# Kernel optimization log

Measured on AMD Instinct MI355X. Metric: run time of the kernel, lower is better.

The kernel has to match this reference:

```python
import jax, jax.numpy as jnp
import numpy as np

N, F, DEG, C = 20000, 64, 16, 16   # nodes, features, in-degree incl. self loop, classes
E = N * (DEG - 1)                   # regular (non-self-loop) edges


def setup_inputs() -> dict:
    key = jax.random.key(0)
    ks = jax.random.split(key, 12)
    x = jax.random.normal(ks[0], (N, F), dtype=jnp.float32)
    src = jax.random.randint(ks[1], (E,), 0, N, dtype=jnp.int32)
    dst = jnp.repeat(jnp.arange(N, dtype=jnp.int32), DEG - 1)  # exactly DEG-1 in-edges/node
    edge_index = jnp.stack([src, dst])
    s = 1.0 / np.sqrt(F)
    params = {}
    for i, kw, kb in ((1, ks[2], ks[3]), (2, ks[4], ks[5]), (3, ks[6], ks[7])):
        params[f"W{i}"] = jax.random.normal(kw, (F, F), dtype=jnp.float32) * s
        params[f"b{i}"] = jax.random.normal(kb, (F,), dtype=jnp.float32) * s
    params["Wfc"] = jax.random.normal(ks[8], (C, F), dtype=jnp.float32) * s
    params["bfc"] = jax.random.normal(ks[9], (C,), dtype=jnp.float32) * s
    return {"x": x, "edge_index": edge_index, **params}


def _pca_conv(h, src, dst, W, b):
    # GCNConv.forward: linear first, then propagate with symmetric normalization.
    hl = h @ W.T                                             # [N, F]
    # add self loops (appended after regular edges, as in PyG)
    loop = jnp.arange(N, dtype=src.dtype)
    src_a = jnp.concatenate([src, loop])
    dst_a = jnp.concatenate([dst, loop])
    deg = jnp.zeros((N,), hl.dtype).at[dst_a].add(1.0)
    dinv = jax.lax.rsqrt(deg)
    norm = dinv[src_a] * dinv[dst_a]                         # [Ea]
    m = norm[:, None] * hl[src_a]                            # messages [Ea, F]
    # aggregate(): pack each destination's messages contiguously, in edge order
    order = jnp.argsort(dst_a)                               # stable sort by destination
    sd = dst_a[order]
    slot = jnp.arange(sd.shape[0]) - jnp.searchsorted(sd, sd, side='left')
    neigh = jnp.zeros((N, DEG, F), hl.dtype).at[sd, slot].set(m[order])
    neigh = neigh.reshape(N, DEG * F)                        # [N, max_degree*F]
    # torch.pca_lowrank(neigh, q=F, center=True): top-F right singular vectors of
    # the column-centered matrix; computed via eigh on the (DEG*F x DEG*F) Gram.
    Xc = neigh - jnp.mean(neigh, axis=0, keepdims=True)
    G = Xc.T @ Xc                                            # [DEG*F, DEG*F]
    _, V = jnp.linalg.eigh(G)                                # ascending eigenvalues
    Vtop = V[:, ::-1][:, :F]                                 # top-F principal directions
    proj = neigh @ Vtop                                      # note: projects UNcentered neigh
    return proj @ W.T + b                                    # self.lin again + bias


def reference(x, edge_index, W1, b1, W2, b2, W3, b3, Wfc, bfc):
    src, dst = edge_index[0], edge_index[1]
    h = jax.nn.relu(_pca_conv(x, src, dst, W1, b1))
    h = jax.nn.relu(_pca_conv(h, src, dst, W2, b2))
    h = jax.nn.relu(_pca_conv(h, src, dst, W3, b3))
    out = h @ Wfc.T + bfc
    return jax.nn.log_softmax(out, axis=-1)
```

## Files before the change

### kernel.cpp

```cpp
#include <hip/hip_runtime.h>
#include <cmath>

#define NNODES 20000
#define FD 64
#define EPN 15
#define NB 1024
#define BSUB 80
#define NCLS 16
#define SYRK_SPLIT 16

__global__ __launch_bounds__(256) void k_linT(const float* __restrict__ X,
    const float* __restrict__ W, const float* __restrict__ bias,
    float* __restrict__ out, int ncol, int relu)
{
  __shared__ float Wsh[64][65];
  __shared__ float Xsh[64][65];
  int t = threadIdx.x;
  int r0 = blockIdx.x * 64;
  for (int idx = t; idx < ncol * 64; idx += 256) Wsh[idx >> 6][idx & 63] = W[idx];
  for (int idx = t; idx < 64 * 64; idx += 256) {
    int r = idx >> 6, c = idx & 63;
    Xsh[r][c] = (r0 + r < NNODES) ? X[(size_t)(r0 + r) * 64 + c] : 0.f;
  }
  __syncthreads();
  for (int idx = t; idx < 64 * ncol; idx += 256) {
    int r = idx / ncol, o = idx % ncol;
    float acc = 0.f;
    #pragma unroll
    for (int j = 0; j < 64; j++) acc += Xsh[r][j] * Wsh[o][j];
    if (bias) acc += bias[o];
    if (relu) acc = fmaxf(acc, 0.f);
    if (r0 + r < NNODES) out[(size_t)(r0 + r) * ncol + o] = acc;
  }
}

__global__ __launch_bounds__(256) void k_meanslot(const float* __restrict__ hl,
    const int* __restrict__ src, float* __restrict__ mus)
{
  int k = blockIdx.x;
  int part = blockIdx.y;
  int t = threadIdx.x;
  int c = t & 63, sub = t >> 6;
  int d0 = part * 2500;
  float acc = 0.f;
  for (int d = d0 + sub; d < d0 + 2500; d += 4) {
    int row = (k < EPN) ? src[d * EPN + k] : d;
    acc += hl[(size_t)row * 64 + c];
  }
  __shared__ float red[4][64];
  red[sub][c] = acc;
  __syncthreads();
  if (t < 64) {
    float s = red[0][t] + red[1][t] + red[2][t] + red[3][t];
    atomicAdd(&mus[k * 64 + t], s * (1.f / 20000.f));
  }
}

__global__ __launch_bounds__(256) void k_buildX(const float* __restrict__ hl,
    const int* __restrict__ src, const float* __restrict__ mus,
    float* __restrict__ X)
{
  __shared__ float4 mu4[256];
  int t = threadIdx.x;
  int d0 = blockIdx.x * 64;
  mu4[t] = ((const float4*)mus)[t];
  __syncthreads();
  for (int k = 0; k < 16; k++) {
    for (int item = t; item < 1024; item += 256) {
      int rr = item >> 4, f4 = item & 15;
      int d = d0 + rr;
      if (d < NNODES) {
        int row = (k < EPN) ? src[d * EPN + k] : d;
        float4 v = ((const float4*)hl)[(size_t)row * 16 + f4];
        float4 m = mu4[k * 16 + f4];
        v.x -= m.x; v.y -= m.y; v.z -= m.z; v.w -= m.w;
        ((float4*)X)[(size_t)d * 256 + k * 16 + f4] = v;
      }
    }
  }
}

__global__ __launch_bounds__(256) void k_syrkX(const float* __restrict__ X,
    float* __restrict__ TP)
{
  __shared__ float As[32][128];
  __shared__ float Bs[32][128];
  int t = threadIdx.x;
  int pr = blockIdx.x, I = 0, rem = pr;
  for (int ii = 0; ii < 8; ii++) {
    int cnt = 8 - ii;
    if (rem < cnt) { I = ii; break; }
    rem -= cnt;
  }
  int J = I + rem;
  int d0 = blockIdx.y * (NNODES / SYRK_SPLIT);
  int d1 = d0 + (NNODES / SYRK_SPLIT);
  int a0 = (t & 15) * 8, b0 = (t >> 4) * 8;
  float acc[8][8] = {};
  for (int dc = d0; dc < d1; dc += 32) {
    __syncthreads();
    for (int item = t; item < 1024; item += 256) {
      int rr = item >> 5, c4 = item & 31;
      int d = dc + rr;
      float4 va = make_float4(0.f, 0.f, 0.f, 0.f), vb = va;
      if (d < d1) {
        va = ((const float4*)X)[(size_t)d * 256 + I * 32 + c4];
        vb = ((const float4*)X)[(size_t)d * 256 + J * 32 + c4];
      }
      *(float4*)&As[rr][c4 * 4] = va;
      *(float4*)&Bs[rr][c4 * 4] = vb;
    }
    __syncthreads();
    for (int dd = 0; dd < 32; dd++) {
      float av[8], bv[8];
      *(float4*)&av[0] = *(const float4*)&As[dd][a0];
      *(float4*)&av[4] = *(const float4*)&As[dd][a0 + 4];
      *(float4*)&bv[0] = *(const float4*)&Bs[dd][b0];
      *(float4*)&bv[4] = *(const float4*)&Bs[dd][b0 + 4];
      #pragma unroll
      for (int x = 0; x < 8; x++)
        #pragma unroll
        for (int y = 0; y < 8; y++) acc[x][y] += av[x] * bv[y];
    }
  }
  float* Tout = TP + (size_t)blockIdx.y * ((size_t)NB * NB);
  #pragma unroll
  for (int x = 0; x < 8; x++) {
    size_t base = (size_t)(I * 128 + a0 + x) * NB + (J * 128 + b0);
    *(float4*)&Tout[base]     = make_float4(acc[x][0], acc[x][1], acc[x][2], acc[x][3]);
    *(float4*)&Tout[base + 4] = make_float4(acc[x][4], acc[x][5], acc[x][6], acc[x][7]);
  }
}

__global__ __launch_bounds__(256) void k_assembleG16(const float* __restrict__ TP,
    float* __restrict__ G)
{
  size_t idx = (size_t)blockIdx.x * 256 + threadIdx.x;
  int p = (int)(idx >> 10), q = (int)(idx & 1023);
  int ti = p >> 6, tj = q >> 6;
  size_t e = (ti <= tj) ? idx : (((size_t)q << 10) | (size_t)p);
  float v = 0.f;
  #pragma unroll
  for (int s2 = 0; s2 < 16; s2++) v += TP[(size_t)s2 * ((size_t)NB * NB) + e];
  G[idx] = v * (1.f / 256.f);
}

__global__ __launch_bounds__(256) void k_gram(const float* __restrict__ hl,
    const int* __restrict__ src, const float* __restrict__ mus,
    float* __restrict__ T)
{
  __shared__ float Ash[64][64];
  __shared__ float Bsh[64][64];
  __shared__ float muA[64], muB[64];
  int t = threadIdx.x;
  int pr = blockIdx.x, i = 0, rem = pr;
  for (int ii = 0; ii < 16; ii++) {
    int cnt = 16 - ii;
    if (rem < cnt) { i = ii; break; }
    rem -= cnt;
  }
  int j = i + rem;
  if (t < 64) muA[t] = mus[i * 64 + t];
  else if (t < 128) muB[t - 64] = mus[j * 64 + (t - 64)];
  float acc[4][4] = {};
  int a0 = (t & 15) * 4, b0 = (t >> 4) * 4;
  int d0 = blockIdx.y * 4000, d1 = d0 + 4000;
  for (int dc = d0; dc < d1; dc += 64) {
    __syncthreads();
    for (int item = t; item < 1024; item += 256) {
      int rr = item >> 4, f4 = item & 15;
      int d = dc + rr;
      float4 va = make_float4(0.f, 0.f, 0.f, 0.f);
      float4 vb = va;
      if (d < d1) {
        int ra = (i < EPN) ? src[d * EPN + i] : d;
        int rb = (j < EPN) ? src[d * EPN + j] : d;
        va = ((const float4*)hl)[(size_t)ra * 16 + f4];
        vb = ((const float4*)hl)[(size_t)rb * 16 + f4];
        int cb = f4 * 4;
        va.x -= muA[cb]; va.y -= muA[cb + 1]; va.z -= muA[cb + 2]; va.w -= muA[cb + 3];
        vb.x -= muB[cb]; vb.y -= muB[cb + 1]; vb.z -= muB[cb + 2]; vb.w -= muB[cb + 3];
      }
      ((float4*)&Ash[rr][0])[f4] = va;
      ((float4*)&Bsh[rr][0])[f4] = vb;
    }
    __syncthreads();
    for (int dd = 0; dd < 64; dd++) {
      float av[4], bv[4];
      #pragma unroll
      for (int u = 0; u < 4; u++) av[u] = Ash[dd][a0 + u];
      #pragma unroll
      for (int u = 0; u < 4; u++) bv[u] = Bsh[dd][b0 + u];
      #pragma unroll
      for (int x = 0; x < 4; x++)
        #pragma unroll
        for (int y = 0; y < 4; y++) acc[x][y] += av[x] * bv[y];
// ... 114 lines not shown
    }
    __syncthreads();
    for (int kk = 0; kk < 64; kk++) {
      float g0 = Gs[rg * 2 + 0][kk];
      float g1 = Gs[rg * 2 + 1][kk];
      float z[5];
      #pragma unroll
      for (int m = 0; m < 5; m++) z[m] = Zs[kk][cg * 5 + m];
      #pragma unroll
      for (int m = 0; m < 5; m++) { acc0[m] += g0 * z[m]; acc1[m] += g1 * z[m]; }
    }
  }
  size_t base = (size_t)kz * (NB * BSUB) + (size_t)(r0 + rg * 2) * BSUB + cg * 5;
  #pragma unroll
  for (int m = 0; m < 5; m++) P[base + m] = acc0[m];
  #pragma unroll
  for (int m = 0; m < 5; m++) P[base + BSUB + m] = acc1[m];
  __threadfence();
  __syncthreads();
  if (t == 0) {
    int old = atomicAdd(&cnt[r0b], 1);
    lastf = (old == 7) ? 1 : 0;
  }
  __syncthreads();
  if (!lastf) return;
  __threadfence();
  float coef = s1;
  if (cptr) coef = s1 * (float)(2.0 / cptr[0]);
  const float4* P4 = (const float4*)P;
  for (int idx = t; idx < 640; idx += 256) {
    size_t o4 = (size_t)r0 * 20 + idx;
    float4 a = P4[o4];
    #pragma unroll
    for (int u = 1; u < 8; u++) {
      float4 b = P4[(size_t)u * 20480 + o4];
      a.x += b.x; a.y += b.y; a.z += b.z; a.w += b.w;
    }
    float4 z = ((const float4*)Z)[o4];
    float4 o;
    o.x = coef * a.x + s2 * z.x;
    o.y = coef * a.y + s2 * z.y;
    o.z = coef * a.z + s2 * z.z;
    o.w = coef * a.w + s2 * z.w;
    if (s3 != 0.f) {
      float4 zp = ((const float4*)Zp)[o4];
      o.x += s3 * zp.x; o.y += s3 * zp.y; o.z += s3 * zp.z; o.w += s3 * zp.w;
    }
    ((float4*)out)[o4] = o;
  }
  __syncthreads();
  if (t == 0) cnt[r0b] = 0;
}

__global__ void k_syrk(const float* __restrict__ S, double* __restrict__ C)
{
  int idx = blockIdx.x * 256 + threadIdx.x;
  if (idx >= BSUB * BSUB) return;
  int a = idx / BSUB, b = idx % BSUB;
  double acc = 0.0;
  for (int i = 0; i < NB; i++)
    acc += (double)S[(size_t)i * BSUB + a] * (double)S[(size_t)i * BSUB + b];
  C[idx] = acc;
}

__global__ void k_xty(const float* __restrict__ X, const float* __restrict__ Y,
                      float* __restrict__ M)
{
  int idx = blockIdx.x * 256 + threadIdx.x;
  if (idx >= BSUB * BSUB) return;
  int a = idx / BSUB, b = idx % BSUB;
  double acc = 0.0;
  for (int i = 0; i < NB; i++)
    acc += (double)X[(size_t)i * BSUB + a] * (double)Y[(size_t)i * BSUB + b];
  M[idx] = (float)acc;
}

__global__ __launch_bounds__(512) void k_cholinv(const double* __restrict__ Cin,
    float* __restrict__ Rinv)
{
  __shared__ double R[BSUB][BSUB + 1];
  __shared__ double rownew[2][BSUB];
  __shared__ double dinv[BSUB];
  __shared__ float X[BSUB][BSUB + 1];
  int t = threadIdx.x;
  for (int idx = t; idx < BSUB * BSUB; idx += 512)
    R[idx / BSUB][idx % BSUB] = Cin[idx];
  __syncthreads();
  double flr0 = 1e-30 * (fabs(R[0][0]) + 1e-280);
  int prevrow = -1;
  int pb = 0;
  int k = 0;
  while (k < BSUB - 1) {
    int nrem = BSUB - 1 - k;
    int total = (nrem * (nrem + 1)) >> 1;
    int cplen = (prevrow >= 0) ? (BSUB - prevrow) : 0;
    double piv = R[k][k];
    if (piv < flr0) piv = flr0;
    double rp = 1.0 / piv;
    bool pair = (k + 1 < BSUB - 1);
    if (pair) {
      double dk1 = R[k][k + 1];
      double p1 = R[k + 1][k + 1] - dk1 * dk1 * rp;
      if (p1 < flr0) p1 = flr0;
      double rp1 = 1.0 / p1;
      for (int idx = t; idx < total + cplen; idx += 512) {
        if (idx < total) {
          float nf = 2.f * (float)nrem + 1.f;
          int a = (int)((nf - sqrtf(nf * nf - 8.f * (float)idx)) * 0.5f);
          while (a > 0 && a * nrem - ((a * (a - 1)) >> 1) > idx) a--;
          while ((a + 1) * nrem - (((a + 1) * a) >> 1) <= idx) a++;
          int off = idx - (a * nrem - ((a * (a - 1)) >> 1));
          int i2 = k + 1 + a, j2 = i2 + off;
          if (a == 0) {
            rownew[pb][j2] = R[k + 1][j2] - dk1 * R[k][j2] * rp;
          } else {
            double v = R[i2][j2] - R[k][i2] * R[k][j2] * rp;
            double R1i = R[k + 1][i2] - dk1 * R[k][i2] * rp;
            double R1j = R[k + 1][j2] - dk1 * R[k][j2] * rp;
            v -= R1i * R1j * rp1;
            R[i2][j2] = v;
          }
        } else {
          int j = prevrow + (idx - total);
          R[prevrow][j] = rownew[pb ^ 1][j];
        }
      }
      __syncthreads();
      prevrow = k + 1; pb ^= 1; k += 2;
    } else {
      for (int idx = t; idx < total + cplen; idx += 512) {
        if (idx < total) {
          float nf = 2.f * (float)nrem + 1.f;
          int a = (int)((nf - sqrtf(nf * nf - 8.f * (float)idx)) * 0.5f);
          while (a > 0 && a * nrem - ((a * (a - 1)) >> 1) > idx) a--;
          while ((a + 1) * nrem - (((a + 1) * a) >> 1) <= idx) a++;
          int off = idx - (a * nrem - ((a * (a - 1)) >> 1));
          int i2 = k + 1 + a, j2 = i2 + off;
          R[i2][j2] -= R[k][i2] * R[k][j2] * rp;
        } else {
// ... 8 lines not shown
  if (prevrow >= 0) {
    for (int j = prevrow + t; j < BSUB; j += 512) R[prevrow][j] = rownew[pb ^ 1][j];
    __syncthreads();
  }
  if (t < BSUB) {
    double piv = R[t][t];
    if (piv < flr0) piv = flr0;
    dinv[t] = 1.0 / sqrt(piv);
  }
  __syncthreads();
  for (int idx = t; idx < BSUB * BSUB; idx += 512) {
    int kk = idx / BSUB, j = idx % BSUB;
    if (j > kk) R[kk][j] *= dinv[kk];
  }
  __syncthreads();
  if (t < BSUB) R[t][t] = 1.0 / dinv[t];
  __syncthreads();
  if (t < BSUB) {
    int j = t;
    X[j][j] = (float)dinv[j];
    for (int i = j - 1; i >= 0; i--) {
      double s = 0.0;
      for (int k2 = i + 1; k2 <= j; k2++) s += R[i][k2] * (double)X[k2][j];
      X[i][j] = (float)(-s * dinv[i]);
    }
    for (int i = j + 1; i < BSUB; i++) X[i][j] = 0.f;
  }
  __syncthreads();
  for (int idx = t; idx < BSUB * BSUB; idx += 512)
    Rinv[idx] = X[idx / BSUB][idx % BSUB];
}

__global__ __launch_bounds__(256) void k_gemmSR(const float* __restrict__ S,
    const float* __restrict__ Rinv, float* __restrict__ out)
{
  __shared__ float Rsh[BSUB][84];
  int t = threadIdx.x;
  for (int idx = t; idx < BSUB * BSUB; idx += 256)
    Rsh[idx / BSUB][idx % BSUB] = Rinv[idx];
  __syncthreads();
  int r0 = blockIdx.x * 32;
  int r = t >> 3, c0 = (t & 7) * 10;
  float acc[10] = {};
  const float* srow = &S[(size_t)(r0 + r) * BSUB];
  for (int k = 0; k < BSUB; k++) {
    float s = srow[k];
    #pragma unroll
    for (int m = 0; m < 10; m++) acc[m] += s * Rsh[k][c0 + m];
  }
  #pragma unroll
  for (int m = 0; m < 10; m++) out[(size_t)(r0 + r) * BSUB + c0 + m] = acc[m];
}

__global__ __launch_bounds__(1024) void k_jacobi(const float* __restrict__ Min,
    float* __restrict__ Uout, int* __restrict__ perm,
    double* __restrict__ cutout, int sweeps, int withU)
{
  __shared__ float Mb[2][BSUB][BSUB + 1];
  __shared__ float Ut[BSUB][BSUB];
  __shared__ float4 rot[2][40];
  __shared__ float th[BSUB];
  __shared__ int id[BSUB];
  int t = threadIdx.x;
  for (int idx = t; idx < BSUB * BSUB; idx += 1024) {
    int i2 = idx / BSUB, j2 = idx % BSUB;
    Mb[0][i2][j2] = 0.5f * (Min[i2 * BSUB + j2] + Min[j2 * BSUB + i2]);
    if (withU) Ut[i2][j2] = (i2 == j2) ? 1.f : 0.f;
  }
  int pr0 = t / 40, j0 = t - pr0 * 40;
  int pr1 = -1, j1 = 0;
  {
    int i1 = t + 1024;
    if (i1 < 1600) { pr1 = i1 / 40; j1 = i1 - pr1 * 40; }
  }
  int upr0 = -1, um0 = 0, upr1 = -1, um1 = 0;
  if (t >= 40) {
    int u0 = t - 40;              upr0 = u0 / 40; um0 = u0 - upr0 * 40;
    int u1 = t - 40 + 984;
    if (u1 < 1600) { upr1 = u1 / 40; um1 = u1 - upr1 * 40; }
  }
  int rp_ = 0, rq_ = 0;
  if (t < 40) {
    rp_ = (t == 0) ? 0 : 1 + (t - 1) % 79;
    rq_ = 1 + (78 - t) % 79;
  }
  __syncthreads();
  int nrounds = sweeps * (BSUB - 1);
  int mcur = 0;
  for (int it = 0; it < nrounds; it++) {
    int pb = it & 1;
    float (*Mc)[BSUB + 1] = Mb[mcur];
    float (*Mn)[BSUB + 1] = Mb[mcur ^ 1];
    if (t < 40) {
      int p = rp_, q = rq_;
      if (p > q) { int tmp = p; p = q; q = tmp; }
      float apq = Mc[p][q];
      float c = 1.f, s = 0.f;
      if (fabsf(apq) > 1e-28f) {
        float tau = (Mc[q][q] - Mc[p][p]) / (2.f * apq);
        float tt = copysignf(1.f, tau) / (fabsf(tau) + sqrtf(1.f + tau * tau));
        c = rsqrtf(1.f + tt * tt);
        s = tt * c;
      }
      rot[pb][t] = make_float4(c, s, __int_as_float(p), __int_as_float(q));
      if (t > 0) rp_ = (rp_ == 79) ? 1 : rp_ + 1;
      rq_ = (rq_ == 79) ? 1 : rq_ + 1;
    } else if (withU && it > 0) {
      int ob = pb ^ 1;
      {
        float4 R0 = rot[ob][upr0];
        int p = __float_as_int(R0.z), q = __float_as_int(R0.w);
        float c = R0.x, s = R0.y;
        float2 up = *(float2*)&Ut[p][2 * um0];
        float2 uq = *(float2*)&Ut[q][2 * um0];
        float2 np, nq;
        np.x = c * up.x - s * uq.x;  np.y = c * up.y - s * uq.y;
        nq.x = s * up.x + c * uq.x;  nq.y = s * up.y + c * uq.y;
        *(float2*)&Ut[p][2 * um0] = np;
        *(float2*)&Ut[q][2 * um0] = nq;
      }
      if (upr1 >= 0) {
        float4 R1 = rot[ob][upr1];
        int p = __float_as_int(R1.z), q = __float_as_int(R1.w);
        float c = R1.x, s = R1.y;
        float2 up = *(float2*)&Ut[p][2 * um1];
        float2 uq = *(float2*)&Ut[q][2 * um1];
        float2 np, nq;
        np.x = c * up.x - s * uq.x;  np.y = c * up.y - s * uq.y;
        nq.x = s * up.x + c * uq.x;  nq.y = s * up.y + c * uq.y;
        *(float2*)&Ut[p][2 * um1] = np;
        *(float2*)&Ut[q][2 * um1] = nq;
      }
    }
    __syncthreads();
    {
      float4 Rp = rot[pb][pr0];
      float4 Rj = rot[pb][j0];
      int p = __float_as_int(Rp.z), q = __float_as_int(Rp.w);
      float c = Rp.x, s = Rp.y;
      int k = __float_as_int(Rj.z), k2 = __float_as_int(Rj.w);
      float cj = Rj.x, sj = Rj.y;
      float mpk = Mc[p][k],  mqk = Mc[q][k];
      float mpk2 = Mc[p][k2], mqk2 = Mc[q][k2];
      float rpk  = c * mpk  - s * mqk;
      float rqk  = s * mpk  + c * mqk;
      float rpk2 = c * mpk2 - s * mqk2;
      float rqk2 = s * mpk2 + c * mqk2;
      Mn[p][k]  = cj * rpk - sj * rpk2;
      Mn[q][k]  = cj * rqk - sj * rqk2;
      Mn[p][k2] = sj * rpk + cj * rpk2;
      Mn[q][k2] = sj * rqk + cj * rqk2;
    }
    if (pr1 >= 0) {
      float4 Rp = rot[pb][pr1];
      float4 Rj = rot[pb][j1];
      int p = __float_as_int(Rp.z), q = __float_as_int(Rp.w);
      float c = Rp.x, s = Rp.y;
      int k = __float_as_int(Rj.z), k2 = __float_as_int(Rj.w);
      float cj = Rj.x, sj = Rj.y;
      float mpk = Mc[p][k],  mqk = Mc[q][k];
      float mpk2 = Mc[p][k2], mqk2 = Mc[q][k2];
      float rpk  = c * mpk  - s * mqk;
      float rqk  = s * mpk  + c * mqk;
      float rpk2 = c * mpk2 - s * mqk2;
      float rqk2 = s * mpk2 + c * mqk2;
      Mn[p][k]  = cj * rpk - sj * rpk2;
      Mn[q][k]  = cj * rqk - sj * rqk2;
      Mn[p][k2] = sj * rpk + cj * rpk2;
      Mn[q][k2] = sj * rqk + cj * rqk2;
    }
    __syncthreads();
    mcur ^= 1;
  }
  if (withU) {
    int ob = (nrounds - 1) & 1;
    {
      float4 R0 = rot[ob][pr0];
      int p = __float_as_int(R0.z), q = __float_as_int(R0.w);
      float c = R0.x, s = R0.y;
      float2 up = *(float2*)&Ut[p][2 * j0];
      float2 uq = *(float2*)&Ut[q][2 * j0];
      float2 np, nq;
      np.x = c * up.x - s * uq.x;  np.y = c * up.y - s * uq.y;
      nq.x = s * up.x + c * uq.x;  nq.y = s * up.y + c * uq.y;
      *(float2*)&Ut[p][2 * j0] = np;
      *(float2*)&Ut[q][2 * j0] = nq;
    }
    if (pr1 >= 0) {
      float4 R1 = rot[ob][pr1];
      int p = __float_as_int(R1.z), q = __float_as_int(R1.w);
      float c = R1.x, s = R1.y;
      float2 up = *(float2*)&Ut[p][2 * j1];
      float2 uq = *(float2*)&Ut[q][2 * j1];
      float2 np, nq;
      np.x = c * up.x - s * uq.x;  np.y = c * up.y - s * uq.y;
      nq.x = s * up.x + c * uq.x;  nq.y = s * up.y + c * uq.y;
      *(float2*)&Ut[p][2 * j1] = np;
      *(float2*)&Ut[q][2 * j1] = nq;
    }
    __syncthreads();
  }
  float (*Mf)[BSUB + 1] = Mb[mcur];
  if (t < BSUB) { th[t] = Mf[t][t]; id[t] = t; }
  __syncthreads();
  if (t == 0) {
    for (int a = 1; a < BSUB; a++) {
      float v = th[a]; int ii = id[a]; int b = a - 1;
      while (b >= 0 && th[b] < v) { th[b + 1] = th[b]; id[b + 1] = id[b]; b--; }
      th[b + 1] = v; id[b + 1] = ii;
    }
    double cut = (double)th[BSUB - 1];
    double lo = 0.02 * (double)th[0];
    if (cut < lo) cut = lo;
    double hi = 0.98 * (double)th[63];
    if (cut > hi) cut = hi;
    cutout[0] = cut;
    cutout[1] = cut * cut;
  }
  __syncthreads();
  if (t < BSUB) perm[t] = id[t];
  if (withU)
    for (int idx = t; idx < BSUB * BSUB; idx += 1024) {
      int k = idx / BSUB, p = idx % BSUB;
      Uout[idx] = Ut[p][k];
    }
}

__global__ __launch_bounds__(256) void k_compose(const float* __restrict__ S,
    const float* __restrict__ U, const int* __restrict__ perm,
    float* __restrict__ out)
{
  __shared__ float Ush[BSUB][65];
  int t = threadIdx.x;
  for (int idx = t; idx < BSUB * 64; idx += 256) {
    int jj = idx >> 6, c = idx & 63;
    Ush[jj][c] = U[jj * BSUB + perm[c]];
  }
  __syncthreads();
  int r0 = blockIdx.x * 64;
  for (int oidx = t; oidx < 64 * 64; oidx += 256) {
    int r = oidx >> 6, c = oidx & 63;
    float acc = 0.f;
    const float* srow = &S[(size_t)(r0 + r) * BSUB];
    #pragma unroll 8
    for (int j = 0; j < BSUB; j++) acc += srow[j] * Ush[j][c];
    out[(size_t)(r0 + r) * 64 + c] = acc;
  }
}

__global__ __launch_bounds__(256) void k_projlin(const float* __restrict__ hl,
    const int* __restrict__ src, const float* __restrict__ Vtop,
// ... 40 lines not shown
    for (int m = 0; m < 16; m++) {
      int o = pg * 16 + m;
      float a = bias[o];
      for (int j = 0; j < 64; j++) a += Psh[dd][j] * Vsh[o][j];
      hout[(size_t)(d0 + dd) * 64 + o] = fmaxf(a, 0.f);
    }
  }
}

__global__ void k_logsoftmax(const float* __restrict__ logits, float* __restrict__ out)
{
  int n = blockIdx.x * 256 + threadIdx.x;
  if (n >= NNODES) return;
  float v[NCLS];
  float mx = -1e30f;
  #pragma unroll
  for (int c = 0; c < NCLS; c++) { v[c] = logits[(size_t)n * NCLS + c]; mx = fmaxf(mx, v[c]); }
  float se = 0.f;
  #pragma unroll
  for (int c = 0; c < NCLS; c++) se += expf(v[c] - mx);
  float lse = mx + logf(se);
  #pragma unroll
  for (int c = 0; c < NCLS; c++) out[(size_t)n * NCLS + c] = v[c] - lse;
}

extern "C" void kernel_launch(void* const* d_in, const int* in_sizes, int n_in,
                              void* d_out, int out_size, void* d_ws, size_t ws_size,
                              hipStream_t stream)
{
  (void)in_sizes; (void)n_in; (void)out_size;
  const float* x = (const float*)d_in[0];
  const int* src = (const int*)d_in[1];
  const float* Wl[3] = { (const float*)d_in[2], (const float*)d_in[4], (const float*)d_in[6] };
  const float* bl[3] = { (const float*)d_in[3], (const float*)d_in[5], (const float*)d_in[7] };
  const float* Wfc = (const float*)d_in[8];
  const float* bfc = (const float*)d_in[9];
  float* outp = (float*)d_out;

  char* w = (char*)d_ws;
  auto alloc = [&](size_t bytes) -> char* {
    char* p = w; w += (bytes + 255) & ~(size_t)255; return p;
  };
  float* hA   = (float*)alloc((size_t)NNODES * 64 * 4);
  float* hB   = (float*)alloc((size_t)NNODES * 64 * 4);
  float* hl   = (float*)alloc((size_t)NNODES * 64 * 4);
  float* T    = (float*)alloc((size_t)NB * NB * 4);
  float* G    = (float*)alloc((size_t)NB * NB * 4);
  float* G2   = (float*)alloc((size_t)NB * NB * 4);
  float* mus  = (float*)alloc(16 * 64 * 4);
  float* Zb[6];
  for (int i = 0; i < 6; i++) Zb[i] = (float*)alloc((size_t)NB * BSUB * 4);
  float* P     = (float*)alloc((size_t)8 * NB * BSUB * 4);
  int* cnt     = (int*)alloc(32 * 4);
  double* C    = (double*)alloc(BSUB * BSUB * 8);
  float* Rinv  = (float*)alloc(BSUB * BSUB * 4);
  float* Mm    = (float*)alloc(BSUB * BSUB * 4);
  float* U     = (float*)alloc(BSUB * BSUB * 4);
  int* perm    = (int*)alloc(BSUB * 4);
  float* Vtop  = (float*)alloc((size_t)NB * 64 * 4);
  double* scal = (double*)alloc(16 * 8);
  float* X  = (float*)alloc((size_t)NNODES * NB * 4);
  float* TP = (float*)alloc((size_t)SYRK_SPLIT * (size_t)NB * NB * 4);
  size_t used = (size_t)(w - (char*)d_ws);
  int fastg = (used <= ws_size) ? 1 : 0;

  const int GRID_ROWS = (NNODES + 63) / 64;

  hipMemsetAsync(cnt, 0, 32 * 4, stream);

  int cur = 0;
  auto gemmGZ = [&](const float* A, const float* Z, const float* Zp, float* o,
                    const double* cptr, float s1, float s2, float s3) {
    hipLaunchKernelGGL(k_gzfused, dim3(32, 8), dim3(256), 0, stream,
                       A, Z, Zp, P, o, cnt, cptr, s1, s2, s3);
  };
  auto chunk2 = [&](int deg, const double* cptr) {
    int a = (cur + 1) % 6, b = (cur + 2) % 6;
    float* bufs[3] = { Zb[cur], Zb[a], Zb[b] };
    int ip = 0, ic = 0, io = 1;
    for (int s = 0; s < deg; s++) {
      if (s == 0)
        gemmGZ(G2, bufs[ic], nullptr, bufs[io], cptr, 1.f, -1.f, 0.f);
      else
        gemmGZ(G2, bufs[ic], bufs[ip], bufs[io], cptr, 2.f, -2.f, -1.f);
      if (s == 0) { ip = 0; ic = 1; io = 2; }
      else { int tmp = ip; ip = ic; ic = io; io = tmp; }
    }
    int sel = (deg - 1) % 3;
    cur = (sel == 0) ? a : (sel == 1) ? b : cur;
  };
  auto cholqr = [&]() {
    hipLaunchKernelGGL(k_syrk, dim3(25), dim3(256), 0, stream, Zb[cur], C);
    hipLaunchKernelGGL(k_cholinv, dim3(1), dim3(512), 0, stream, C, Rinv);
    int o = (cur + 1) % 6;
    hipLaunchKernelGGL(k_gemmSR, dim3(32), dim3(256), 0, stream, Zb[cur], Rinv, Zb[o]);
    cur = o;
  };
  auto rrmid = [&](double* cutp) {
    int y = (cur + 1) % 6;
    gemmGZ(G, Zb[cur], nullptr, Zb[y], nullptr, 1.f, 0.f, 0.f);
    hipLaunchKernelGGL(k_xty, dim3(25), dim3(256), 0, stream, Zb[cur], Zb[y], Mm);
    hipLaunchKernelGGL(k_jacobi, dim3(1), dim3(1024), 0, stream,
                       Mm, U, perm, cutp, 2, 0);
  };
  auto rrfinal = [&](double* cutp) {
    int y = (cur + 1) % 6;
    gemmGZ(G, Zb[cur], nullptr, Zb[y], nullptr, 1.f, 0.f, 0.f);
    hipLaunchKernelGGL(k_xty, dim3(25), dim3(256), 0, stream, Zb[cur], Zb[y], Mm);
    hipLaunchKernelGGL(k_jacobi, dim3(1), dim3(1024), 0, stream,
                       Mm, U, perm, cutp, 5, 1);
    hipLaunchKernelGGL(k_compose, dim3(16), dim3(256), 0, stream,
                       Zb[cur], U, perm, Vtop);
  };

  const float* hin = x;
  float* hout = hA;
  for (int l = 0; l < 3; l++) {
    hipLaunchKernelGGL(k_linT, dim3(GRID_ROWS), dim3(256), 0, stream,
                       hin, Wl[l], (const float*)nullptr, hl, 64, 0);
    hipMemsetAsync(mus, 0, 16 * 64 * 4, stream);
    hipLaunchKernelGGL(k_meanslot, dim3(16, 8), dim3(256), 0, stream, hl, src, mus);
    if (fastg) {
      hipLaunchKernelGGL(k_buildX, dim3(GRID_ROWS), dim3(256), 0, stream,
                         hl, src, mus, X);
      hipLaunchKernelGGL(k_syrkX, dim3(36, SYRK_SPLIT), dim3(256), 0, stream, X, TP);
      hipLaunchKernelGGL(k_assembleG16, dim3(4096), dim3(256), 0, stream, TP, G);
    } else {
      hipMemsetAsync(T, 0, (size_t)NB * NB * 4, stream);
      hipLaunchKernelGGL(k_gram, dim3(136, 5), dim3(256), 0, stream, hl, src, mus, T);
      hipLaunchKernelGGL(k_assembleG, dim3(4096), dim3(256), 0, stream, T, G);
    }
    hipLaunchKernelGGL(k_cut0, dim3(1), dim3(256), 0, stream, G, scal);
    hipLaunchKernelGGL(k_gemmG2, dim3(16, 16), dim3(256), 0, stream, G, G2);
    cur = 0;
    hipLaunchKernelGGL(k_initS, dim3((NB * BSUB + 255) / 256), dim3(256), 0, stream, Zb[cur]);
    chunk2(6, &scal[1]); cholqr();
    rrmid(&scal[2]);
    chunk2(7, &scal[3]); cholqr();
    chunk2(7, &scal[3]); cholqr();
    rrfinal(&scal[4]);
    hipLaunchKernelGGL(k_projlin, dim3(GRID_ROWS), dim3(256), 0, stream,
                       hl, src, Vtop, Wl[l], bl[l], hout);
    hin = hout;
    hout = (hout == hA) ? hB : hA;
  }
  hipLaunchKernelGGL(k_linT, dim3(GRID_ROWS), dim3(256), 0, stream,
                     hin, Wfc, bfc, hl, NCLS, 0);
  hipLaunchKernelGGL(k_logsoftmax, dim3((NNODES + 255) / 256), dim3(256), 0, stream,
                     hl, outp);
}
```

Before: 9.352 ms.

## Tile the small Gram products and merge Jacobi rotation phases into one pass

Replaces the naive per-element 80x80 Gram kernels, which each loop serially over all 1024 rows, with a shared-memory tiled kernel. Each of its 16 blocks computes a 5x5 register tile per thread over 64 rows and writes its own fp64 partial. The 16 partials are summed when the Cholesky and Jacobi kernels load their input. The Jacobi kernel is also restructured: each of 820 threads now computes both rotation pairs itself and updates a symmetric 2x2 block, which removes one barrier per round. The U update now uses float4 vectors. The risk is redundant rotation-angle computation per thread and a changed summation order.

```diff
diff --git a/kernel.cpp b/kernel.cpp
--- a/kernel.cpp
+++ b/kernel.cpp
@@ -8,6 +8,8 @@
 #define BSUB 80
 #define NCLS 16
 #define SYRK_SPLIT 16
+#define NPAIR 40
+#define NTRI 820
 
 __global__ __launch_bounds__(256) void k_linT(const float* __restrict__ X,
     const float* __restrict__ W, const float* __restrict__ bias,
@@ -362,27 +364,38 @@
   if (t == 0) cnt[r0b] = 0;
 }
 
-__global__ void k_syrk(const float* __restrict__ S, double* __restrict__ C)
-{
-  int idx = blockIdx.x * 256 + threadIdx.x;
-  if (idx >= BSUB * BSUB) return;
-  int a = idx / BSUB, b = idx % BSUB;
-  double acc = 0.0;
-  for (int i = 0; i < NB; i++)
-    acc += (double)S[(size_t)i * BSUB + a] * (double)S[(size_t)i * BSUB + b];
-  C[idx] = acc;
-}
-
-__global__ void k_xty(const float* __restrict__ X, const float* __restrict__ Y,
-                      float* __restrict__ M)
-{
-  int idx = blockIdx.x * 256 + threadIdx.x;
-  if (idx >= BSUB * BSUB) return;
-  int a = idx / BSUB, b = idx % BSUB;
-  double acc = 0.0;
-  for (int i = 0; i < NB; i++)
-    acc += (double)X[(size_t)i * BSUB + a] * (double)Y[(size_t)i * BSUB + b];
-  M[idx] = (float)acc;
+__global__ __launch_bounds__(256) void k_xty2(const float* __restrict__ X,
+    const float* __restrict__ Y, double* __restrict__ CP)
+{
+  __shared__ float Xsh[64][BSUB + 1];
+  __shared__ float Ysh[64][BSUB + 1];
+  int t = threadIdx.x;
+  int i0 = blockIdx.x * 64;
+  for (int idx = t; idx < 64 * BSUB; idx += 256) {
+    int r = idx / BSUB, c = idx % BSUB;
+    Xsh[r][c] = X[(size_t)(i0 + r) * BSUB + c];
+    Ysh[r][c] = Y[(size_t)(i0 + r) * BSUB + c];
+  }
+  __syncthreads();
+  int a0 = (t & 15) * 5, b0 = (t >> 4) * 5;
+  double acc[5][5] = {};
+  for (int dd = 0; dd < 64; dd++) {
+    float av[5], bv[5];
+    #pragma unroll
+    for (int u = 0; u < 5; u++) av[u] = Xsh[dd][a0 + u];
+    #pragma unroll
+    for (int u = 0; u < 5; u++) bv[u] = Ysh[dd][b0 + u];
+    #pragma unroll
+    for (int x = 0; x < 5; x++)
+      #pragma unroll
+      for (int y = 0; y < 5; y++) acc[x][y] += (double)av[x] * (double)bv[y];
+  }
+  double* out = CP + (size_t)blockIdx.x * (BSUB * BSUB);
+  #pragma unroll
+  for (int x = 0; x < 5; x++)
+    #pragma unroll
+    for (int y = 0; y < 5; y++)
+      out[(size_t)(a0 + x) * BSUB + (b0 + y)] = acc[x][y];
 }
 
 __global__ __launch_bounds__(512) void k_cholinv(const double* __restrict__ Cin,
@@ -393,8 +406,12 @@
   __shared__ double dinv[BSUB];
   __shared__ float X[BSUB][BSUB + 1];
   int t = threadIdx.x;
-  for (int idx = t; idx < BSUB * BSUB; idx += 512)
-    R[idx / BSUB][idx % BSUB] = Cin[idx];
+  for (int idx = t; idx < BSUB * BSUB; idx += 512) {
+    double s = 0.0;
+    #pragma unroll
+    for (int b = 0; b < 16; b++) s += Cin[(size_t)b * (BSUB * BSUB) + idx];
+    R[idx / BSUB][idx % BSUB] = s;
+  }
   __syncthreads();
   double flr0 = 1e-30 * (fabs(R[0][0]) + 1e-280);
   int prevrow = -1;
@@ -509,37 +526,37 @@
   for (int m = 0; m < 10; m++) out[(size_t)(r0 + r) * BSUB + c0 + m] = acc[m];
 }
 
-__global__ __launch_bounds__(1024) void k_jacobi(const float* __restrict__ Min,
+__global__ __launch_bounds__(1024) void k_jacobi(const double* __restrict__ Min,
     float* __restrict__ Uout, int* __restrict__ perm,
     double* __restrict__ cutout, int sweeps, int withU)
 {
   __shared__ float Mb[2][BSUB][BSUB + 1];
-  __shared__ float Ut[BSUB][BSUB];
-  __shared__ float4 rot[2][40];
+  __shared__ __align__(16) float Ut[BSUB][BSUB];
+  __shared__ float4 rot[2][NPAIR];
   __shared__ float th[BSUB];
   __shared__ int id[BSUB];
   int t = threadIdx.x;
   for (int idx = t; idx < BSUB * BSUB; idx += 1024) {
+    double s = 0.0;
+    #pragma unroll
+    for (int b = 0; b < 16; b++) s += Min[(size_t)b * (BSUB * BSUB) + idx];
+    Mb[1][idx / BSUB][idx % BSUB] = (float)s;
+    if (withU) Ut[idx / BSUB][idx % BSUB] = ((idx / BSUB) == (idx % BSUB)) ? 1.f : 0.f;
+  }
+  int mi = -1, mj = 0;
+  if (t < NTRI) {
+    int ia = 0, rem = t;
+    while (rem >= NPAIR - ia) { rem -= NPAIR - ia; ia++; }
+    mi = ia; mj = ia + rem;
+  }
+  int upr = -1, um4 = 0;
+  if (t < NPAIR * 20) { upr = t / 20; um4 = t % 20; }
+  int pA_ = mi, qA_ = 79 - mi;
+  int pB_ = mj, qB_ = 79 - mj;
+  __syncthreads();
+  for (int idx = t; idx < BSUB * BSUB; idx += 1024) {
     int i2 = idx / BSUB, j2 = idx % BSUB;
-    Mb[0][i2][j2] = 0.5f * (Min[i2 * BSUB + j2] + Min[j2 * BSUB + i2]);
-    if (withU) Ut[i2][j2] = (i2 == j2) ? 1.f : 0.f;
-  }
-  int pr0 = t / 40, j0 = t - pr0 * 40;
-  int pr1 = -1, j1 = 0;
-  {
-    int i1 = t + 1024;
-    if (i1 < 1600) { pr1 = i1 / 40; j1 = i1 - pr1 * 40; }
-  }
-  int upr0 = -1, um0 = 0, upr1 = -1, um1 = 0;
-  if (t >= 40) {
-    int u0 = t - 40;              upr0 = u0 / 40; um0 = u0 - upr0 * 40;
-    int u1 = t - 40 + 984;
-    if (u1 < 1600) { upr1 = u1 / 40; um1 = u1 - upr1 * 40; }
-  }
-  int rp_ = 0, rq_ = 0;
-  if (t < 40) {
-    rp_ = (t == 0) ? 0 : 1 + (t - 1) % 79;
-    rq_ = 1 + (78 - t) % 79;
+    Mb[0][i2][j2] = 0.5f * (Mb[1][i2][j2] + Mb[1][j2][i2]);
   }
   __syncthreads();
   int nrounds = sweeps * (BSUB - 1);
@@ -548,112 +565,84 @@
     int pb = it & 1;
     float (*Mc)[BSUB + 1] = Mb[mcur];
     float (*Mn)[BSUB + 1] = Mb[mcur ^ 1];
-    if (t < 40) {
-      int p = rp_, q = rq_;
+    if (mi >= 0) {
+      int p = pA_, q = qA_;
       if (p > q) { int tmp = p; p = q; q = tmp; }
-      float apq = Mc[p][q];
-      float c = 1.f, s = 0.f;
-      if (fabsf(apq) > 1e-28f) {
-        float tau = (Mc[q][q] - Mc[p][p]) / (2.f * apq);
-        float tt = copysignf(1.f, tau) / (fabsf(tau) + sqrtf(1.f + tau * tau));
-        c = rsqrtf(1.f + tt * tt);
-        s = tt * c;
+      float cA = 1.f, sA = 0.f;
+      {
+        float apq = Mc[p][q];
+        if (fabsf(apq) > 1e-28f) {
+          float tau = (Mc[q][q] - Mc[p][p]) / (2.f * apq);
+          float tt = copysignf(1.f, tau) / (fabsf(tau) + sqrtf(1.f + tau * tau));
+          cA = rsqrtf(1.f + tt * tt);
+          sA = tt * cA;
+        }
       }
-      rot[pb][t] = make_float4(c, s, __int_as_float(p), __int_as_float(q));
-      if (t > 0) rp_ = (rp_ == 79) ? 1 : rp_ + 1;
-      rq_ = (rq_ == 79) ? 1 : rq_ + 1;
-    } else if (withU && it > 0) {
-      int ob = pb ^ 1;
+      int kk = pB_, k2 = qB_;
+      if (kk > k2) { int tmp = kk; kk = k2; k2 = tmp; }
+      float cB = 1.f, sB = 0.f;
       {
-        float4 R0 = rot[ob][upr0];
-        int p = __float_as_int(R0.z), q = __float_as_int(R0.w);
-        float c = R0.x, s = R0.y;
-        float2 up = *(float2*)&Ut[p][2 * um0];
-        float2 uq = *(float2*)&Ut[q][2 * um0];
-        float2 np, nq;
-        np.x = c * up.x - s * uq.x;  np.y = c * up.y - s * uq.y;
-        nq.x = s * up.x + c * uq.x;  nq.y = s * up.y + c * uq.y;
-        *(float2*)&Ut[p][2 * um0] = np;
-        *(float2*)&Ut[q][2 * um0] = nq;
+        float apq = Mc[kk][k2];
+        if (fabsf(apq) > 1e-28f) {
+          float tau = (Mc[k2][k2] - Mc[kk][kk]) / (2.f * apq);
+          float tt = copysignf(1.f, tau) / (fabsf(tau) + sqrtf(1.f + tau * tau));
+          cB = rsqrtf(1.f + tt * tt);
+          sB = tt * cB;
+        }
       }
-      if (upr1 >= 0) {
-        float4 R1 = rot[ob][upr1];
-        int p = __float_as_int(R1.z), q = __float_as_int(R1.w);
-        float c = R1.x, s = R1.y;
-        float2 up = *(float2*)&Ut[p][2 * um1];
-        float2 uq = *(float2*)&Ut[q][2 * um1];
-        float2 np, nq;
-        np.x = c * up.x - s * uq.x;  np.y = c * up.y - s * uq.y;
-        nq.x = s * up.x + c * uq.x;  nq.y = s * up.y + c * uq.y;
-        *(float2*)&Ut[p][2 * um1] = np;
-        *(float2*)&Ut[q][2 * um1] = nq;
+      if (t < NPAIR)
+        rot[pb][t] = make_float4(cB, sB, __int_as_float(kk), __int_as_float(k2));
+      float mpk = Mc[p][kk],  mqk = Mc[q][kk];
+      float mpk2 = Mc[p][k2], mqk2 = Mc[q][k2];
+      float rpk  = cA * mpk  - sA * mqk;
+      float rqk  = sA * mpk  + cA * mqk;
+      float rpk2 = cA * mpk2 - sA * mqk2;
+      float rqk2 = sA * mpk2 + cA * mqk2;
+      float v00 = cB * rpk - sB * rpk2;
+      float v10 = cB * rqk - sB * rqk2;
+      float v01 = sB * rpk + cB * rpk2;
+      float v11 = sB * rqk + cB * rqk2;
+      Mn[p][kk] = v00; Mn[q][kk] = v10; Mn[p][k2] = v01; Mn[q][k2] = v11;
+      if (mi != mj) {
+        Mn[kk][p] = v00; Mn[kk][q] = v10; Mn[k2][p] = v01; Mn[k2][q] = v11;
       }
     }
-    __syncthreads();
-    {
-      float4 Rp = rot[pb][pr0];
-      float4 Rj = rot[pb][j0];
-      int p = __float_as_int(Rp.z), q = __float_as_int(Rp.w);
-      float c = Rp.x, s = Rp.y;
-      int k = __float_as_int(Rj.z), k2 = __float_as_int(Rj.w);
-      float cj = Rj.x, sj = Rj.y;
-      float mpk = Mc[p][k],  mqk = Mc[q][k];
-      float mpk2 = Mc[p][k2], mqk2 = Mc[q][k2];
-      float rpk  = c * mpk  - s * mqk;
-      float rqk  = s * mpk  + c * mqk;
-      float rpk2 = c * mpk2 - s * mqk2;
-      float rqk2 = s * mpk2 + c * mqk2;
-      Mn[p][k]  = cj * rpk - sj * rpk2;
-      Mn[q][k]  = cj * rqk - sj * rqk2;
-      Mn[p][k2] = sj * rpk + cj * rpk2;
-      Mn[q][k2] = sj * rqk + cj * rqk2;
-    }
-    if (pr1 >= 0) {
-      float4 Rp = rot[pb][pr1];
-      float4 Rj = rot[pb][j1];
-      int p = __float_as_int(Rp.z), q = __float_as_int(Rp.w);
-      float c = Rp.x, s = Rp.y;
-      int k = __float_as_int(Rj.z), k2 = __float_as_int(Rj.w);
-      float cj = Rj.x, sj = Rj.y;
-      float mpk = Mc[p][k],  mqk = Mc[q][k];
-      float mpk2 = Mc[p][k2], mqk2 = Mc[q][k2];
-      float rpk  = c * mpk  - s * mqk;
-      float rqk  = s * mpk  + c * mqk;
-      float rpk2 = c * mpk2 - s * mqk2;
-      float rqk2 = s * mpk2 + c * mqk2;
-      Mn[p][k]  = cj * rpk - sj * rpk2;
-      Mn[q][k]  = cj * rqk - sj * rqk2;
-      Mn[p][k2] = sj * rpk + cj * rpk2;
-      Mn[q][k2] = sj * rqk + cj * rqk2;
-    }
+    if (withU && it > 0 && upr >= 0) {
+      float4 R0 = rot[pb ^ 1][upr];
+      int p = __float_as_int(R0.z), q = __float_as_int(R0.w);
+      float c = R0.x, s = R0.y;
+      float4 up = *(float4*)&Ut[p][4 * um4];
+      float4 uq = *(float4*)&Ut[q][4 * um4];
+      float4 np, nq;
+      np.x = c * up.x - s * uq.x;  np.y = c * up.y - s * uq.y;
+      np.z = c * up.z - s * uq.z;  np.w = c * up.w - s * uq.w;
+      nq.x = s * up.x + c * uq.x;  nq.y = s * up.y + c * uq.y;
+      nq.z = s * up.z + c * uq.z;  nq.w = s * up.w + c * uq.w;
+      *(float4*)&Ut[p][4 * um4] = np;
+      *(float4*)&Ut[q][4 * um4] = nq;
+    }
+    if (mi > 0) pA_ = (pA_ == 79) ? 1 : pA_ + 1;
+    if (mj > 0) pB_ = (pB_ == 79) ? 1 : pB_ + 1;
+    qA_ = (qA_ == 79) ? 1 : qA_ + 1;
+    qB_ = (qB_ == 79) ? 1 : qB_ + 1;
     __syncthreads();
     mcur ^= 1;
   }
   if (withU) {
     int ob = (nrounds - 1) & 1;
-    {
-      float4 R0 = rot[ob][pr0];
+    if (upr >= 0) {
+      float4 R0 = rot[ob][upr];
       int p = __float_as_int(R0.z), q = __float_as_int(R0.w);
       float c = R0.x, s = R0.y;
-      float2 up = *(float2*)&Ut[p][2 * j0];
-      float2 uq = *(float2*)&Ut[q][2 * j0];
-      float2 np, nq;
+      float4 up = *(float4*)&Ut[p][4 * um4];
+      float4 uq = *(float4*)&Ut[q][4 * um4];
+      float4 np, nq;
       np.x = c * up.x - s * uq.x;  np.y = c * up.y - s * uq.y;
+      np.z = c * up.z - s * uq.z;  np.w = c * up.w - s * uq.w;
       nq.x = s * up.x + c * uq.x;  nq.y = s * up.y + c * uq.y;
-      *(float2*)&Ut[p][2 * j0] = np;
-      *(float2*)&Ut[q][2 * j0] = nq;
-    }
-    if (pr1 >= 0) {
-      float4 R1 = rot[ob][pr1];
-      int p = __float_as_int(R1.z), q = __float_as_int(R1.w);
-      float c = R1.x, s = R1.y;
-      float2 up = *(float2*)&Ut[p][2 * j1];
-      float2 uq = *(float2*)&Ut[q][2 * j1];
-      float2 np, nq;
-      np.x = c * up.x - s * uq.x;  np.y = c * up.y - s * uq.y;
-      nq.x = s * up.x + c * uq.x;  nq.y = s * up.y + c * uq.y;
-      *(float2*)&Ut[p][2 * j1] = np;
-      *(float2*)&Ut[q][2 * j1] = nq;
+      nq.z = s * up.z + c * uq.z;  nq.w = s * up.w + c * uq.w;
+      *(float4*)&Ut[p][4 * um4] = np;
+      *(float4*)&Ut[q][4 * um4] = nq;
     }
     __syncthreads();
   }
@@ -800,9 +789,8 @@
   for (int i = 0; i < 6; i++) Zb[i] = (float*)alloc((size_t)NB * BSUB * 4);
   float* P     = (float*)alloc((size_t)8 * NB * BSUB * 4);
   int* cnt     = (int*)alloc(32 * 4);
-  double* C    = (double*)alloc(BSUB * BSUB * 8);
+  double* CP   = (double*)alloc((size_t)16 * BSUB * BSUB * 8);
   float* Rinv  = (float*)alloc(BSUB * BSUB * 4);
-  float* Mm    = (float*)alloc(BSUB * BSUB * 4);
   float* U     = (float*)alloc(BSUB * BSUB * 4);
   int* perm    = (int*)alloc(BSUB * 4);
   float* Vtop  = (float*)alloc((size_t)NB * 64 * 4);
@@ -838,8 +826,8 @@
     cur = (sel == 0) ? a : (sel == 1) ? b : cur;
   };
   auto cholqr = [&]() {
-    hipLaunchKernelGGL(k_syrk, dim3(25), dim3(256), 0, stream, Zb[cur], C);
-    hipLaunchKernelGGL(k_cholinv, dim3(1), dim3(512), 0, stream, C, Rinv);
+    hipLaunchKernelGGL(k_xty2, dim3(16), dim3(256), 0, stream, Zb[cur], Zb[cur], CP);
+    hipLaunchKernelGGL(k_cholinv, dim3(1), dim3(512), 0, stream, CP, Rinv);
     int o = (cur + 1) % 6;
     hipLaunchKernelGGL(k_gemmSR, dim3(32), dim3(256), 0, stream, Zb[cur], Rinv, Zb[o]);
     cur = o;
@@ -847,16 +835,16 @@
   auto rrmid = [&](double* cutp) {
     int y = (cur + 1) % 6;
     gemmGZ(G, Zb[cur], nullptr, Zb[y], nullptr, 1.f, 0.f, 0.f);
-    hipLaunchKernelGGL(k_xty, dim3(25), dim3(256), 0, stream, Zb[cur], Zb[y], Mm);
+    hipLaunchKernelGGL(k_xty2, dim3(16), dim3(256), 0, stream, Zb[cur], Zb[y], CP);
     hipLaunchKernelGGL(k_jacobi, dim3(1), dim3(1024), 0, stream,
-                       Mm, U, perm, cutp, 2, 0);
+                       CP, U, perm, cutp, 2, 0);
   };
   auto rrfinal = [&](double* cutp) {
     int y = (cur + 1) % 6;
     gemmGZ(G, Zb[cur], nullptr, Zb[y], nullptr, 1.f, 0.f, 0.f);
-    hipLaunchKernelGGL(k_xty, dim3(25), dim3(256), 0, stream, Zb[cur], Zb[y], Mm);
+    hipLaunchKernelGGL(k_xty2, dim3(16), dim3(256), 0, stream, Zb[cur], Zb[y], CP);
     hipLaunchKernelGGL(k_jacobi, dim3(1), dim3(1024), 0, stream,
-                       Mm, U, perm, cutp, 5, 1);
+                       CP, U, perm, cutp, 5, 1);
     hipLaunchKernelGGL(k_compose, dim3(16), dim3(256), 0, stream,
                        Zb[cur], U, perm, Vtop);
   };
```

New measurement: 9.976 ms. +6.7%, slower.

## Parallelize small Gram products, split-reduce into Cholesky/Jacobi, retune SYRK split

Applied to the files above, without the earlier changes.

Replaces the naive per-element double-precision k_syrk and k_xty kernels with a tiled shared-memory k_xty2. It splits the 1024-row reduction across 16 blocks and writes 16 partial products, which k_cholinv and k_jacobi now sum on load. The main SYRK can now split into 20 row slices when workspace allows, and its thread-to-tile mapping is changed to strided 4+4 column groups to reduce LDS bank conflicts. The cost is a slightly larger workspace and extra partial-sum reads inside the single-block kernels.

```diff
diff --git a/kernel.cpp b/kernel.cpp
--- a/kernel.cpp
+++ b/kernel.cpp
@@ -7,7 +7,7 @@
 #define NB 1024
 #define BSUB 80
 #define NCLS 16
-#define SYRK_SPLIT 16
+#define NPAIR 40
 
 __global__ __launch_bounds__(256) void k_linT(const float* __restrict__ X,
     const float* __restrict__ W, const float* __restrict__ bias,
@@ -81,7 +81,7 @@
 }
 
 __global__ __launch_bounds__(256) void k_syrkX(const float* __restrict__ X,
-    float* __restrict__ TP)
+    float* __restrict__ TP, int rows)
 {
   __shared__ float As[32][128];
   __shared__ float Bs[32][128];
@@ -93,9 +93,9 @@
     rem -= cnt;
   }
   int J = I + rem;
-  int d0 = blockIdx.y * (NNODES / SYRK_SPLIT);
-  int d1 = d0 + (NNODES / SYRK_SPLIT);
-  int a0 = (t & 15) * 8, b0 = (t >> 4) * 8;
+  int d0 = blockIdx.y * rows;
+  int d1 = d0 + rows;
+  int a0 = (t & 15) * 4, b0 = (t >> 4) * 4;
   float acc[8][8] = {};
   for (int dc = d0; dc < d1; dc += 32) {
     __syncthreads();
@@ -114,9 +114,9 @@
     for (int dd = 0; dd < 32; dd++) {
       float av[8], bv[8];
       *(float4*)&av[0] = *(const float4*)&As[dd][a0];
-      *(float4*)&av[4] = *(const float4*)&As[dd][a0 + 4];
+      *(float4*)&av[4] = *(const float4*)&As[dd][a0 + 64];
       *(float4*)&bv[0] = *(const float4*)&Bs[dd][b0];
-      *(float4*)&bv[4] = *(const float4*)&Bs[dd][b0 + 4];
+      *(float4*)&bv[4] = *(const float4*)&Bs[dd][b0 + 64];
       #pragma unroll
       for (int x = 0; x < 8; x++)
         #pragma unroll
@@ -126,22 +126,22 @@
   float* Tout = TP + (size_t)blockIdx.y * ((size_t)NB * NB);
   #pragma unroll
   for (int x = 0; x < 8; x++) {
-    size_t base = (size_t)(I * 128 + a0 + x) * NB + (J * 128 + b0);
-    *(float4*)&Tout[base]     = make_float4(acc[x][0], acc[x][1], acc[x][2], acc[x][3]);
-    *(float4*)&Tout[base + 4] = make_float4(acc[x][4], acc[x][5], acc[x][6], acc[x][7]);
+    int rowi = I * 128 + ((x < 4) ? (a0 + x) : (64 + a0 + x - 4));
+    size_t base = (size_t)rowi * NB + J * 128;
+    *(float4*)&Tout[base + b0]      = make_float4(acc[x][0], acc[x][1], acc[x][2], acc[x][3]);
+    *(float4*)&Tout[base + 64 + b0] = make_float4(acc[x][4], acc[x][5], acc[x][6], acc[x][7]);
   }
 }
 
 __global__ __launch_bounds__(256) void k_assembleG16(const float* __restrict__ TP,
-    float* __restrict__ G)
+    float* __restrict__ G, int ns)
 {
   size_t idx = (size_t)blockIdx.x * 256 + threadIdx.x;
   int p = (int)(idx >> 10), q = (int)(idx & 1023);
   int ti = p >> 6, tj = q >> 6;
   size_t e = (ti <= tj) ? idx : (((size_t)q << 10) | (size_t)p);
   float v = 0.f;
-  #pragma unroll
-  for (int s2 = 0; s2 < 16; s2++) v += TP[(size_t)s2 * ((size_t)NB * NB) + e];
+  for (int s2 = 0; s2 < ns; s2++) v += TP[(size_t)s2 * ((size_t)NB * NB) + e];
   G[idx] = v * (1.f / 256.f);
 }
 
@@ -362,27 +362,38 @@
   if (t == 0) cnt[r0b] = 0;
 }
 
-__global__ void k_syrk(const float* __restrict__ S, double* __restrict__ C)
-{
-  int idx = blockIdx.x * 256 + threadIdx.x;
-  if (idx >= BSUB * BSUB) return;
-  int a = idx / BSUB, b = idx % BSUB;
-  double acc = 0.0;
-  for (int i = 0; i < NB; i++)
-    acc += (double)S[(size_t)i * BSUB + a] * (double)S[(size_t)i * BSUB + b];
-  C[idx] = acc;
-}
-
-__global__ void k_xty(const float* __restrict__ X, const float* __restrict__ Y,
-                      float* __restrict__ M)
-{
-  int idx = blockIdx.x * 256 + threadIdx.x;
-  if (idx >= BSUB * BSUB) return;
-  int a = idx / BSUB, b = idx % BSUB;
-  double acc = 0.0;
-  for (int i = 0; i < NB; i++)
-    acc += (double)X[(size_t)i * BSUB + a] * (double)Y[(size_t)i * BSUB + b];
-  M[idx] = (float)acc;
+__global__ __launch_bounds__(256) void k_xty2(const float* __restrict__ X,
+    const float* __restrict__ Y, double* __restrict__ CP)
+{
+  __shared__ float Xsh[64][BSUB + 1];
+  __shared__ float Ysh[64][BSUB + 1];
+  int t = threadIdx.x;
+  int i0 = blockIdx.x * 64;
+  for (int idx = t; idx < 64 * BSUB; idx += 256) {
+    int r = idx / BSUB, c = idx % BSUB;
+    Xsh[r][c] = X[(size_t)(i0 + r) * BSUB + c];
+    Ysh[r][c] = Y[(size_t)(i0 + r) * BSUB + c];
+  }
+  __syncthreads();
+  int a0 = (t & 15) * 5, b0 = (t >> 4) * 5;
+  double acc[5][5] = {};
+  for (int dd = 0; dd < 64; dd++) {
+    float av[5], bv[5];
+    #pragma unroll
+    for (int u = 0; u < 5; u++) av[u] = Xsh[dd][a0 + u];
+    #pragma unroll
+    for (int u = 0; u < 5; u++) bv[u] = Ysh[dd][b0 + u];
+    #pragma unroll
+    for (int x = 0; x < 5; x++)
+      #pragma unroll
+      for (int y = 0; y < 5; y++) acc[x][y] += (double)av[x] * (double)bv[y];
+  }
+  double* out = CP + (size_t)blockIdx.x * (BSUB * BSUB);
+  #pragma unroll
+  for (int x = 0; x < 5; x++)
+    #pragma unroll
+    for (int y = 0; y < 5; y++)
+      out[(size_t)(a0 + x) * BSUB + (b0 + y)] = acc[x][y];
 }
 
 __global__ __launch_bounds__(512) void k_cholinv(const double* __restrict__ Cin,
@@ -393,8 +404,12 @@
   __shared__ double dinv[BSUB];
   __shared__ float X[BSUB][BSUB + 1];
   int t = threadIdx.x;
-  for (int idx = t; idx < BSUB * BSUB; idx += 512)
-    R[idx / BSUB][idx % BSUB] = Cin[idx];
+  for (int idx = t; idx < BSUB * BSUB; idx += 512) {
+    double s = 0.0;
+    #pragma unroll
+    for (int b = 0; b < 16; b++) s += Cin[(size_t)b * (BSUB * BSUB) + idx];
+    R[idx / BSUB][idx % BSUB] = s;
+  }
   __syncthreads();
   double flr0 = 1e-30 * (fabs(R[0][0]) + 1e-280);
   int prevrow = -1;
@@ -509,20 +524,22 @@
   for (int m = 0; m < 10; m++) out[(size_t)(r0 + r) * BSUB + c0 + m] = acc[m];
 }
 
-__global__ __launch_bounds__(1024) void k_jacobi(const float* __restrict__ Min,
+__global__ __launch_bounds__(1024) void k_jacobi(const double* __restrict__ Min,
     float* __restrict__ Uout, int* __restrict__ perm,
     double* __restrict__ cutout, int sweeps, int withU)
 {
   __shared__ float Mb[2][BSUB][BSUB + 1];
   __shared__ float Ut[BSUB][BSUB];
-  __shared__ float4 rot[2][40];
+  __shared__ float4 rot[2][NPAIR];
   __shared__ float th[BSUB];
   __shared__ int id[BSUB];
   int t = threadIdx.x;
   for (int idx = t; idx < BSUB * BSUB; idx += 1024) {
-    int i2 = idx / BSUB, j2 = idx % BSUB;
-    Mb[0][i2][j2] = 0.5f * (Min[i2 * BSUB + j2] + Min[j2 * BSUB + i2]);
-    if (withU) Ut[i2][j2] = (i2 == j2) ? 1.f : 0.f;
+    double s = 0.0;
+    #pragma unroll
+    for (int b = 0; b < 16; b++) s += Min[(size_t)b * (BSUB * BSUB) + idx];
+    Mb[1][idx / BSUB][idx % BSUB] = (float)s;
+    if (withU) Ut[idx / BSUB][idx % BSUB] = ((idx / BSUB) == (idx % BSUB)) ? 1.f : 0.f;
   }
   int pr0 = t / 40, j0 = t - pr0 * 40;
   int pr1 = -1, j1 = 0;
@@ -540,6 +557,11 @@
   if (t < 40) {
     rp_ = (t == 0) ? 0 : 1 + (t - 1) % 79;
     rq_ = 1 + (78 - t) % 79;
+  }
+  __syncthreads();
+  for (int idx = t; idx < BSUB * BSUB; idx += 1024) {
+    int i2 = idx / BSUB, j2 = idx % BSUB;
+    Mb[0][i2][j2] = 0.5f * (Mb[1][i2][j2] + Mb[1][j2][i2]);
   }
   __syncthreads();
   int nrounds = sweeps * (BSUB - 1);
@@ -800,17 +822,19 @@
   for (int i = 0; i < 6; i++) Zb[i] = (float*)alloc((size_t)NB * BSUB * 4);
   float* P     = (float*)alloc((size_t)8 * NB * BSUB * 4);
   int* cnt     = (int*)alloc(32 * 4);
-  double* C    = (double*)alloc(BSUB * BSUB * 8);
+  double* CP   = (double*)alloc((size_t)16 * BSUB * BSUB * 8);
   float* Rinv  = (float*)alloc(BSUB * BSUB * 4);
-  float* Mm    = (float*)alloc(BSUB * BSUB * 4);
   float* U     = (float*)alloc(BSUB * BSUB * 4);
   int* perm    = (int*)alloc(BSUB * 4);
   float* Vtop  = (float*)alloc((size_t)NB * 64 * 4);
   double* scal = (double*)alloc(16 * 8);
-  float* X  = (float*)alloc((size_t)NNODES * NB * 4);
-  float* TP = (float*)alloc((size_t)SYRK_SPLIT * (size_t)NB * NB * 4);
-  size_t used = (size_t)(w - (char*)d_ws);
-  int fastg = (used <= ws_size) ? 1 : 0;
+  float* X      = (float*)alloc((size_t)NNODES * NB * 4);
+  float* TP     = (float*)alloc((size_t)16 * (size_t)NB * NB * 4);
+  size_t used16 = (size_t)(w - (char*)d_ws);
+  (void)alloc((size_t)4 * (size_t)NB * NB * 4);
+  size_t used20 = (size_t)(w - (char*)d_ws);
+  int fastg = (used16 <= ws_size) ? 1 : 0;
+  int NS    = (used20 <= ws_size) ? 20 : 16;
 
   const int GRID_ROWS = (NNODES + 63) / 64;
 
@@ -838,8 +862,8 @@
     cur = (sel == 0) ? a : (sel == 1) ? b : cur;
   };
   auto cholqr = [&]() {
-    hipLaunchKernelGGL(k_syrk, dim3(25), dim3(256), 0, stream, Zb[cur], C);
-    hipLaunchKernelGGL(k_cholinv, dim3(1), dim3(512), 0, stream, C, Rinv);
+    hipLaunchKernelGGL(k_xty2, dim3(16), dim3(256), 0, stream, Zb[cur], Zb[cur], CP);
+    hipLaunchKernelGGL(k_cholinv, dim3(1), dim3(512), 0, stream, CP, Rinv);
     int o = (cur + 1) % 6;
     hipLaunchKernelGGL(k_gemmSR, dim3(32), dim3(256), 0, stream, Zb[cur], Rinv, Zb[o]);
     cur = o;
@@ -847,16 +871,16 @@
   auto rrmid = [&](double* cutp) {
     int y = (cur + 1) % 6;
     gemmGZ(G, Zb[cur], nullptr, Zb[y], nullptr, 1.f, 0.f, 0.f);
-    hipLaunchKernelGGL(k_xty, dim3(25), dim3(256), 0, stream, Zb[cur], Zb[y], Mm);
+    hipLaunchKernelGGL(k_xty2, dim3(16), dim3(256), 0, stream, Zb[cur], Zb[y], CP);
     hipLaunchKernelGGL(k_jacobi, dim3(1), dim3(1024), 0, stream,
-                       Mm, U, perm, cutp, 2, 0);
+                       CP, U, perm, cutp, 2, 0);
   };
   auto rrfinal = [&](double* cutp) {
     int y = (cur + 1) % 6;
     gemmGZ(G, Zb[cur], nullptr, Zb[y], nullptr, 1.f, 0.f, 0.f);
-    hipLaunchKernelGGL(k_xty, dim3(25), dim3(256), 0, stream, Zb[cur], Zb[y], Mm);
+    hipLaunchKernelGGL(k_xty2, dim3(16), dim3(256), 0, stream, Zb[cur], Zb[y], CP);
     hipLaunchKernelGGL(k_jacobi, dim3(1), dim3(1024), 0, stream,
-                       Mm, U, perm, cutp, 5, 1);
+                       CP, U, perm, cutp, 5, 1);
     hipLaunchKernelGGL(k_compose, dim3(16), dim3(256), 0, stream,
                        Zb[cur], U, perm, Vtop);
   };
@@ -871,8 +895,9 @@
     if (fastg) {
       hipLaunchKernelGGL(k_buildX, dim3(GRID_ROWS), dim3(256), 0, stream,
                          hl, src, mus, X);
-      hipLaunchKernelGGL(k_syrkX, dim3(36, SYRK_SPLIT), dim3(256), 0, stream, X, TP);
-      hipLaunchKernelGGL(k_assembleG16, dim3(4096), dim3(256), 0, stream, TP, G);
+      hipLaunchKernelGGL(k_syrkX, dim3(36, NS), dim3(256), 0, stream,
+                         X, TP, NNODES / NS);
+      hipLaunchKernelGGL(k_assembleG16, dim3(4096), dim3(256), 0, stream, TP, G, NS);
     } else {
       hipMemsetAsync(T, 0, (size_t)NB * NB * 4, stream);
       hipLaunchKernelGGL(k_gram, dim3(136, 5), dim3(256), 0, stream, hl, src, mus, T);
```

New measurement: 8.878 ms. -5.1%, faster.
